# Optimization experiments

Measured on AMD Instinct MI355X. Metric: run time of the kernel, lower is better.

## Reference

```python
import jax, jax.numpy as jnp
import numpy as np

B, S, D = 1, 4096, 512
H, DK, DV = 8, 64, 64


def setup_inputs() -> dict:
    key = jax.random.key(0)
    ks = jax.random.split(key, 8)
    s = 1.0 / np.sqrt(D)
    return {
        "queries": jax.random.normal(ks[0], (B, S, D), jnp.float32),
        "keys": jax.random.normal(ks[1], (B, S, D), jnp.float32),
        "values": jax.random.normal(ks[2], (B, S, D), jnp.float32),
        # Linear weights stored as [in, out] for x @ W
        "Wq": jax.random.normal(ks[3], (D, H * DK), jnp.float32) * s,
        "Wk": jax.random.normal(ks[4], (D, H * DK), jnp.float32) * s,
        "Wv": jax.random.normal(ks[5], (D, H * DV), jnp.float32) * s,
        "Wo": jax.random.normal(ks[6], (H * DV, D), jnp.float32) * s,
        "bo": jax.random.normal(ks[7], (D,), jnp.float32) * 0.02,
    }


def reference(queries, keys, values, Wq, Wk, Wv, Wo, bo):
    b, qlen = values.shape[0], queries.shape[1]
    q = (queries @ Wq).reshape(b, qlen, H, DK)
    k = (keys @ Wk).reshape(b, keys.shape[1], H, DK)
    v = (values @ Wv).reshape(b, values.shape[1], H, DV)
    scale = DK ** 0.5
    # naive full attention: materialize [b, h, sq, sk] scores
    scores = jnp.einsum("bqhd,bkhd->bhqk", q, k) / scale
    attn = jax.nn.softmax(scores, axis=-1)
    out = jnp.einsum("bhqk,bkhd->bqhd", attn, v).reshape(b, qlen, H * DV)
    out = out @ Wo + bo          # first fc_out
    out = out @ Wo + bo          # second fc_out (module applies it twice when not reversible)
    return out
```

## Files before the change

### kernel.cpp

```cpp
#include <hip/hip_runtime.h>

#define S_LEN  4096
#define DMODEL 512
#define NH     8
#define HD     64

typedef _Float16 f16x8 __attribute__((ext_vector_type(8)));
typedef _Float16 f16x4 __attribute__((ext_vector_type(4)));
typedef float    f32x4 __attribute__((ext_vector_type(4)));

static __device__ __forceinline__ unsigned short f2h(float x) {
  return __builtin_bit_cast(unsigned short, (_Float16)x);
}

__global__ __launch_bounds__(256) void wtrans_kernel(
    const float* __restrict__ w0, const float* __restrict__ w1,
    const float* __restrict__ w2, const float* __restrict__ w3,
    unsigned short* __restrict__ o0, unsigned short* __restrict__ o1,
    unsigned short* __restrict__ o2, unsigned short* __restrict__ o3,
    unsigned short* __restrict__ o3s)
{
  __shared__ unsigned short T[64 * 72];
  const float* W; unsigned short* O;
  switch (blockIdx.z) {
    case 0:  W = w0; O = o0; break;
    case 1:  W = w1; O = o1; break;
    case 2:  W = w2; O = o2; break;
    default: W = w3; O = o3; break;
  }
  const int tid = threadIdx.x;
  const int k0 = blockIdx.x * 64, n0 = blockIdx.y * 64;
  const int c4 = (tid & 15) * 4;
#pragma unroll
  for (int rp = 0; rp < 4; ++rp) {
    int r = rp * 16 + (tid >> 4);
    float4 x = *(const float4*)(W + (k0 + r) * DMODEL + n0 + c4);
    T[(c4 + 0) * 72 + r] = f2h(x.x);
    T[(c4 + 1) * 72 + r] = f2h(x.y);
    T[(c4 + 2) * 72 + r] = f2h(x.z);
    T[(c4 + 3) * 72 + r] = f2h(x.w);
    if (blockIdx.z == 3) {
      f16x4 st;
      st[0] = (_Float16)x.x; st[1] = (_Float16)x.y;
      st[2] = (_Float16)x.z; st[3] = (_Float16)x.w;
      *(f16x4*)&o3s[(k0 + r) * DMODEL + n0 + c4] = st;
    }
  }
  __syncthreads();
#pragma unroll
  for (int it = 0; it < 2; ++it) {
    int i = tid + it * 256;
    int nl = i >> 3, c = i & 7;
    *(f16x8*)&O[(n0 + nl) * DMODEL + k0 + c * 8] = *(const f16x8*)&T[nl * 72 + c * 8];
  }
}

__global__ __launch_bounds__(256) void gemm128_kernel(
    const void* __restrict__ A0, const void* __restrict__ A1,
    const void* __restrict__ A2, const void* __restrict__ A3,
    const unsigned short* __restrict__ B0, const unsigned short* __restrict__ B1,
    const unsigned short* __restrict__ B2, const unsigned short* __restrict__ B3,
    void* __restrict__ C0, void* __restrict__ C1,
    void* __restrict__ C2, void* __restrict__ C3,
    const float* __restrict__ bias, unsigned short* __restrict__ vtg,
    const float* __restrict__ wo_f32, const float* __restrict__ bo_in,
    float* __restrict__ bo2_out,
    int a_fp32_mask, int c_fp32_mask)
{
  constexpr int K = DMODEL, N = DMODEL;
  __shared__ unsigned short As[128 * 32];
  __shared__ unsigned short Bs[128 * 32];
  const int z = blockIdx.z;
  if (z == 3 && blockIdx.x >= 4) {
    if (blockIdx.x < 12 && blockIdx.y == 0 && wo_f32) {
      int col = (blockIdx.x - 4) * 64 + (threadIdx.x & 63);
      float s = bo_in[col];
#pragma unroll 8
      for (int j = 0; j < DMODEL; ++j) s = fmaf(bo_in[j], wo_f32[j * DMODEL + col], s);
      bo2_out[col] = s;
    }
    return;
  }
  const void* Av; const unsigned short* Bt; void* Cv;
  switch (z) {
    case 0:  Av = A0; Bt = B0; Cv = C0; break;
    case 1:  Av = A1; Bt = B1; Cv = C1; break;
    case 2:  Av = A2; Bt = B2; Cv = C2; break;
    default: Av = A3; Bt = B3; Cv = C3; break;
  }
  const int a_fp32 = (a_fp32_mask >> z) & 1;
  const int c_fp32 = (c_fp32_mask >> z) & 1;
  const int tid  = threadIdx.x;
  const int lane = tid & 63;
  const int wid  = tid >> 6;
  const int quad = lane >> 4, l16 = lane & 15;
  const int m0 = blockIdx.x * 128, n0 = blockIdx.y * 128;
  const int wm = (wid >> 1) * 64, wn = (wid & 1) * 64;
  f32x4 acc[4][4] = {};

  f16x8 areg[2], breg[2];
#pragma unroll
  for (int it = 0; it < 2; ++it) {
    int s = it * 256 + tid;
    int r = s >> 2, ck = (s & 3) * 8;
    if (a_fp32) {
      const float* p = (const float*)Av + (m0 + r) * K + ck;
      float4 x = *(const float4*)p;
      float4 y = *(const float4*)(p + 4);
      f16x8 av;
      av[0] = (_Float16)x.x; av[1] = (_Float16)x.y;
      av[2] = (_Float16)x.z; av[3] = (_Float16)x.w;
      av[4] = (_Float16)y.x; av[5] = (_Float16)y.y;
      av[6] = (_Float16)y.z; av[7] = (_Float16)y.w;
      areg[it] = av;
    } else {
      areg[it] = *(const f16x8*)((const unsigned short*)Av + (m0 + r) * K + ck);
    }
    breg[it] = *(const f16x8*)(Bt + (n0 + r) * K + ck);
  }

  for (int k0 = 0; k0 < K; k0 += 32) {
    __syncthreads();
#pragma unroll
    for (int it = 0; it < 2; ++it) {
      int s = it * 256 + tid;
      int r = s >> 2, ck = (s & 3) * 8;
      *(f16x8*)&As[r * 32 + ck] = areg[it];
      *(f16x8*)&Bs[r * 32 + ck] = breg[it];
    }
    __syncthreads();

    if (k0 + 32 < K) {
      int kk = k0 + 32;
#pragma unroll
      for (int it = 0; it < 2; ++it) {
        int s = it * 256 + tid;
        int r = s >> 2, ck = (s & 3) * 8;
        if (a_fp32) {
          const float* p = (const float*)Av + (m0 + r) * K + kk + ck;
          float4 x = *(const float4*)p;
          float4 y = *(const float4*)(p + 4);
          f16x8 av;
          av[0] = (_Float16)x.x; av[1] = (_Float16)x.y;
          av[2] = (_Float16)x.z; av[3] = (_Float16)x.w;
          av[4] = (_Float16)y.x; av[5] = (_Float16)y.y;
          av[6] = (_Float16)y.z; av[7] = (_Float16)y.w;
          areg[it] = av;
        } else {
          areg[it] = *(const f16x8*)((const unsigned short*)Av + (m0 + r) * K + kk + ck);
        }
        breg[it] = *(const f16x8*)(Bt + (n0 + r) * K + kk + ck);
      }
    }

    f16x8 af[4], bf[4];
#pragma unroll
    for (int mt = 0; mt < 4; ++mt)
      af[mt] = *(const f16x8*)&As[(wm + mt * 16 + l16) * 32 + quad * 8];
#pragma unroll
    for (int nt = 0; nt < 4; ++nt)
      bf[nt] = *(const f16x8*)&Bs[(wn + nt * 16 + l16) * 32 + quad * 8];
#pragma unroll
    for (int mt = 0; mt < 4; ++mt)
#pragma unroll
      for (int nt = 0; nt < 4; ++nt)
        acc[mt][nt] = __builtin_amdgcn_mfma_f32_16x16x32_f16(af[mt], bf[nt], acc[mt][nt], 0, 0, 0);
  }

  const int do_vt = (vtg != nullptr) && (z == 2);
#pragma unroll
  for (int mt = 0; mt < 4; ++mt)
#pragma unroll
    for (int nt = 0; nt < 4; ++nt) {
      int col = n0 + wn + nt * 16 + l16;
      float bv = bias ? bias[col] : 0.f;
#pragma unroll
      for (int g = 0; g < 4; ++g) {
        int row = m0 + wm + mt * 16 + quad * 4 + g;
        float val = acc[mt][nt][g] + bv;
        if (do_vt)        vtg[col * S_LEN + row] = f2h(val);
        else if (c_fp32)  ((float*)Cv)[row * N + col] = val;
        else              ((unsigned short*)Cv)[row * N + col] = f2h(val);
      }
    }
}

__global__ __launch_bounds__(256) void attn_kernel(
    const unsigned short* __restrict__ Qb, const unsigned short* __restrict__ Kb,
    const unsigned short* __restrict__ VtG,
    float* __restrict__ P0, unsigned short* __restrict__ P1,
    float* __restrict__ mp, float* __restrict__ lp)
{
  __shared__ unsigned short Ks[64 * 72];
  __shared__ unsigned short Vt[64 * 64];

  const int tid  = threadIdx.x;
  const int lane = tid & 63;
  const int wid  = tid >> 6;
  const int quad = lane >> 4, l16 = lane & 15;
  const int qb = blockIdx.x, h = blockIdx.y, z = blockIdx.z;
  const int hc = h * HD;
  const int qbase = qb * 128 + wid * 32;
  const int kz = z * 2048;

  f16x8 bq[2][2];
#pragma unroll
  for (int s = 0; s < 2; ++s) {
    int qrow = qbase + s * 16 + l16;
    bq[s][0] = *(const f16x8*)(Qb + qrow * DMODEL + hc + quad * 8);
    bq[s][1] = *(const f16x8*)(Qb + qrow * DMODEL + hc + 32 + quad * 8);
  }

  f32x4 o[2][4] = {};
  float m_run[2] = {-1e30f, -1e30f}, l_run[2] = {0.f, 0.f};

  f16x8 kreg[2], vreg[2];
#pragma unroll
  for (int it = 0; it < 2; ++it) {
    int s = it * 256 + tid;
    int n = s >> 3, c = s & 7;
    kreg[it] = *(const f16x8*)(Kb + (kz + n) * DMODEL + hc + c * 8);
    vreg[it] = *(const f16x8*)(VtG + (hc + n) * S_LEN + kz + c * 8);
  }

  for (int kbi = 0; kbi < 32; ++kbi) {
    __syncthreads();
#pragma unroll
    for (int it = 0; it < 2; ++it) {
      int s = it * 256 + tid;
      int n = s >> 3, c = s & 7;
      *(f16x8*)&Ks[n * 72 + c * 8] = kreg[it];
      int vbase = n * 16;
      int n15 = n & 15;
      f16x4 lo = __builtin_shufflevector(vreg[it], vreg[it], 0, 1, 2, 3);
      f16x4 hi = __builtin_shufflevector(vreg[it], vreg[it], 4, 5, 6, 7);
      *(f16x4*)&Vt[(vbase + ((2 * c) ^ n15)) * 4]     = lo;
      *(f16x4*)&Vt[(vbase + ((2 * c + 1) ^ n15)) * 4] = hi;
    }
    __syncthreads();

    if (kbi + 1 < 32) {
      int kb1 = kz + (kbi + 1) * 64;
#pragma unroll
      for (int it = 0; it < 2; ++it) {
        int s = it * 256 + tid;
        int n = s >> 3, c = s & 7;
        kreg[it] = *(const f16x8*)(Kb + (kb1 + n) * DMODEL + hc + c * 8);
        vreg[it] = *(const f16x8*)(VtG + (hc + n) * S_LEN + kb1 + c * 8);
      }
    }

    f32x4 sT[2][4];
#pragma unroll
    for (int kt = 0; kt < 4; ++kt) {
      f16x8 ak0 = *(const f16x8*)&Ks[(kt * 16 + l16) * 72 + quad * 8];
      f16x8 ak1 = *(const f16x8*)&Ks[(kt * 16 + l16) * 72 + 32 + quad * 8];
#pragma unroll
      for (int s = 0; s < 2; ++s) {
        f32x4 a = {};
        a = __builtin_amdgcn_mfma_f32_16x16x32_f16(ak0, bq[s][0], a, 0, 0, 0);
        a = __builtin_amdgcn_mfma_f32_16x16x32_f16(ak1, bq[s][1], a, 0, 0, 0);
        sT[s][kt] = a;
      }
    }

    f16x4 pa[2][4];
#pragma unroll
    for (int s = 0; s < 2; ++s) {
      float vmax = -1e30f;
#pragma unroll
      for (int kt = 0; kt < 4; ++kt)
#pragma unroll
        for (int g = 0; g < 4; ++g) vmax = fmaxf(vmax, sT[s][kt][g]);
      vmax = fmaxf(vmax, __shfl_xor(vmax, 16));
      vmax = fmaxf(vmax, __shfl_xor(vmax, 32));

      if (__all(vmax <= m_run[s] + 8.0f)) {
        const float mn = m_run[s];
        float rs = 0.f;
#pragma unroll
        for (int kt = 0; kt < 4; ++kt)
#pragma unroll
          for (int g = 0; g < 4; ++g) {
            float p = __expf((sT[s][kt][g] - mn) * 0.125f);
            rs += p;
            pa[s][kt][g] = (_Float16)p;
          }
        rs += __shfl_xor(rs, 16);
        rs += __shfl_xor(rs, 32);
        l_run[s] += rs;
      } else {
        const float mn = fmaxf(m_run[s], vmax);
        const float alpha = __expf((m_run[s] - mn) * 0.125f);
        m_run[s] = mn;

        float rs = 0.f;
#pragma unroll
        for (int kt = 0; kt < 4; ++kt)
#pragma unroll
          for (int g = 0; g < 4; ++g) {
            float p = __expf((sT[s][kt][g] - mn) * 0.125f);
            rs += p;
            pa[s][kt][g] = (_Float16)p;
          }
        rs += __shfl_xor(rs, 16);
        rs += __shfl_xor(rs, 32);
        l_run[s] = l_run[s] * alpha + rs;

        float ag[4];
#pragma unroll
        for (int g = 0; g < 4; ++g) ag[g] = __shfl(alpha, quad * 4 + g);
#pragma unroll
        for (int nt = 0; nt < 4; ++nt)
#pragma unroll
          for (int g = 0; g < 4; ++g) o[s][nt][g] *= ag[g];
      }
    }

#pragma unroll
    for (int nt = 0; nt < 4; ++nt) {
      int dbase = (nt * 16 + l16) * 16;
#pragma unroll
      for (int kt = 0; kt < 4; ++kt) {
        f16x4 bv = *(const f16x4*)&Vt[(dbase + ((kt * 4 + quad) ^ l16)) * 4];
#pragma unroll
        for (int s = 0; s < 2; ++s)
          o[s][nt] = __builtin_amdgcn_mfma_f32_16x16x16f16(pa[s][kt], bv, o[s][nt], 0, 0, 0);
      }
    }
  }

#pragma unroll
  for (int s = 0; s < 2; ++s) {
    const float lt = l_run[s];
    const float rl = 1.f / lt;
    if (quad == 0) {
      int q = qbase + s * 16 + l16;
      mp[(z * NH + h) * S_LEN + q] = m_run[s];
      lp[(z * NH + h) * S_LEN + q] = lt;
    }
    float rlg[4];
#pragma unroll
    for (int g = 0; g < 4; ++g) rlg[g] = __shfl(rl, quad * 4 + g);
#pragma unroll
    for (int g = 0; g < 4; ++g) {
      int row = qbase + s * 16 + quad * 4 + g;
#pragma unroll
      for (int nt = 0; nt < 4; ++nt) {
        float val = o[s][nt][g] * rlg[g];
        if (z == 0) P0[row * DMODEL + hc + nt * 16 + l16] = val;
        else        P1[row * DMODEL + hc + nt * 16 + l16] = f2h(val);
      }
    }
  }
}

__global__ __launch_bounds__(256) void merge_kernel(
    const float* __restrict__ P0, const unsigned short* __restrict__ P1,
    const float* __restrict__ mp, const float* __restrict__ lp,
    unsigned short* __restrict__ Ob)
{
  const int tid = threadIdx.x;
  const int qb = blockIdx.x, h = blockIdx.y;
  const int q = qb * 64 + (tid >> 2), hc = h * HD;
  const int dq = (tid & 3) * 16;
  const float m0 = mp[h * S_LEN + q],        l0 = lp[h * S_LEN + q];
  const float m1 = mp[(NH + h) * S_LEN + q], l1 = lp[(NH + h) * S_LEN + q];
  const float M  = fmaxf(m0, m1);
  float w0 = l0 * __expf((m0 - M) * 0.125f);
  float w1 = l1 * __expf((m1 - M) * 0.125f);
  const float rw = 1.f / (w0 + w1);
  w0 *= rw; w1 *= rw;
  const int base = q * DMODEL + hc + dq;
  f16x8 p1a = *(const f16x8*)&P1[base];
  f16x8 p1b = *(const f16x8*)&P1[base + 8];
  float4 x0 = *(const float4*)&P0[base];
  float4 x1 = *(const float4*)&P0[base + 4];
  float4 x2 = *(const float4*)&P0[base + 8];
  float4 x3 = *(const float4*)&P0[base + 12];
  f16x8 oa, ob;
  oa[0] = (_Float16)(w0 * x0.x + w1 * (float)p1a[0]);
  oa[1] = (_Float16)(w0 * x0.y + w1 * (float)p1a[1]);
  oa[2] = (_Float16)(w0 * x0.z + w1 * (float)p1a[2]);
  oa[3] = (_Float16)(w0 * x0.w + w1 * (float)p1a[3]);
  oa[4] = (_Float16)(w0 * x1.x + w1 * (float)p1a[4]);
  oa[5] = (_Float16)(w0 * x1.y + w1 * (float)p1a[5]);
  oa[6] = (_Float16)(w0 * x1.z + w1 * (float)p1a[6]);
  oa[7] = (_Float16)(w0 * x1.w + w1 * (float)p1a[7]);
  ob[0] = (_Float16)(w0 * x2.x + w1 * (float)p1b[0]);
  ob[1] = (_Float16)(w0 * x2.y + w1 * (float)p1b[1]);
  ob[2] = (_Float16)(w0 * x2.z + w1 * (float)p1b[2]);
  ob[3] = (_Float16)(w0 * x2.w + w1 * (float)p1b[3]);
  ob[4] = (_Float16)(w0 * x3.x + w1 * (float)p1b[4]);
  ob[5] = (_Float16)(w0 * x3.y + w1 * (float)p1b[5]);
  ob[6] = (_Float16)(w0 * x3.z + w1 * (float)p1b[6]);
  ob[7] = (_Float16)(w0 * x3.w + w1 * (float)p1b[7]);
  *(f16x8*)&Ob[base]     = oa;
  *(f16x8*)&Ob[base + 8] = ob;
}

extern "C" void kernel_launch(void* const* d_in, const int* in_sizes, int n_in,
                              void* d_out, int out_size, void* d_ws, size_t ws_size,
                              hipStream_t stream) {
  const float* q  = (const float*)d_in[0];
  const float* k  = (const float*)d_in[1];
  const float* v  = (const float*)d_in[2];
  const float* Wq = (const float*)d_in[3];
  const float* Wk = (const float*)d_in[4];
  const float* Wv = (const float*)d_in[5];
  const float* Wo = (const float*)d_in[6];
  const float* bo = (const float*)d_in[7];

  unsigned short* ws   = (unsigned short*)d_ws;
  unsigned short* Wqt  = ws;
  unsigned short* Wkt  = Wqt  + 262144;
  unsigned short* Wvt  = Wkt  + 262144;
  unsigned short* Wot  = Wvt  + 262144;
  unsigned short* Wof  = Wot  + 262144;
  unsigned short* Wo2t = Wof  + 262144;
  unsigned short* Qb   = Wo2t + 262144;
  unsigned short* Kb   = Qb   + 2097152;
  unsigned short* VtG  = Kb   + 2097152;
  unsigned short* Ab   = VtG  + 2097152;
  float*          bo2  = (float*)(Ab + 2097152);
  float*          mp   = bo2 + 512;
  float*          lp   = mp + 65536;

  wtrans_kernel<<<dim3(8, 8, 4), 256, 0, stream>>>(
      Wq, Wk, Wv, Wo, Wqt, Wkt, Wvt, Wot, Wof);

  gemm128_kernel<<<dim3(32, 4, 4), 256, 0, stream>>>(
      q, k, v, Wot, Wqt, Wkt, Wvt, Wof, Qb, Kb, nullptr, Wo2t,
      nullptr, VtG, Wo, bo, bo2, 0x7, 0x0);

  attn_kernel<<<dim3(32, 8, 2), 256, 0, stream>>>(
      Qb, Kb, VtG, (float*)d_out, Ab, mp, lp);

  merge_kernel<<<dim3(64, 8), 256, 0, stream>>>(
      (const float*)d_out, Ab, mp, lp, Ab);

  gemm128_kernel<<<dim3(32, 4, 1), 256, 0, stream>>>(
      Ab, nullptr, nullptr, nullptr, Wo2t, nullptr, nullptr, nullptr,
      d_out, nullptr, nullptr, nullptr, bo2, nullptr,
      nullptr, nullptr, nullptr, 0x0, 0x1);
}
```

Measured before the change: 206.6 us.

## Double-buffer attention K/V tiles with direct global-to-LDS loads and XOR swizzle

Replaces the register-staged K/V tile loads in the attention kernel with global_load_lds (direct to LDS) into double-buffered shared tiles. It uses explicit vmcnt waits and raw barriers so the next tile's fetch overlaps the current tile's compute. The padded K layout and the old V swizzle become an XOR-swizzled 64-wide layout, removing register staging and LDS write instructions. The grid is flattened to 1D with heads and splits as the fast index to change block scheduling order, at the cost of hand-managed waitcnt correctness.

```diff
diff --git a/kernel.cpp b/kernel.cpp
--- a/kernel.cpp
+++ b/kernel.cpp
@@ -11,6 +11,12 @@
 
 static __device__ __forceinline__ unsigned short f2h(float x) {
   return __builtin_bit_cast(unsigned short, (_Float16)x);
+}
+
+static __device__ __forceinline__ void glds16(const void* g, void* l) {
+  __builtin_amdgcn_global_load_lds(
+      (const __attribute__((address_space(1))) void*)g,
+      (__attribute__((address_space(3))) void*)l, 16, 0, 0);
 }
 
 __global__ __launch_bounds__(256) void wtrans_kernel(
@@ -191,14 +197,17 @@
     float* __restrict__ P0, unsigned short* __restrict__ P1,
     float* __restrict__ mp, float* __restrict__ lp)
 {
-  __shared__ unsigned short Ks[64 * 72];
-  __shared__ unsigned short Vt[64 * 64];
+  __shared__ unsigned short Ks[2][64 * 64];
+  __shared__ unsigned short Vt[2][64 * 64];
 
   const int tid  = threadIdx.x;
   const int lane = tid & 63;
   const int wid  = tid >> 6;
   const int quad = lane >> 4, l16 = lane & 15;
-  const int qb = blockIdx.x, h = blockIdx.y, z = blockIdx.z;
+  const int id = blockIdx.x;
+  const int qb = id >> 4;
+  const int hz = id & 15;
+  const int h  = hz & 7, z = hz >> 3;
   const int hc = h * HD;
   const int qbase = qb * 128 + wid * 32;
   const int kz = z * 2048;
@@ -210,51 +219,53 @@
     bq[s][0] = *(const f16x8*)(Qb + qrow * DMODEL + hc + quad * 8);
     bq[s][1] = *(const f16x8*)(Qb + qrow * DMODEL + hc + 32 + quad * 8);
   }
+  asm volatile("" : "+v"(bq[0][0]), "+v"(bq[0][1]), "+v"(bq[1][0]), "+v"(bq[1][1]));
 
   f32x4 o[2][4] = {};
   float m_run[2] = {-1e30f, -1e30f}, l_run[2] = {0.f, 0.f};
 
-  f16x8 kreg[2], vreg[2];
-#pragma unroll
-  for (int it = 0; it < 2; ++it) {
-    int s = it * 256 + tid;
-    int n = s >> 3, c = s & 7;
-    kreg[it] = *(const f16x8*)(Kb + (kz + n) * DMODEL + hc + c * 8);
-    vreg[it] = *(const f16x8*)(VtG + (hc + n) * S_LEN + kz + c * 8);
-  }
+  const unsigned short *kp0, *kp1, *vp0, *vp1;
+  {
+    int s0 = tid, s1 = 256 + tid;
+    int n0 = s0 >> 3, c0 = (s0 & 7) ^ (n0 & 7);
+    int n1 = s1 >> 3, c1 = (s1 & 7) ^ (n1 & 7);
+    kp0 = Kb + (kz + n0) * DMODEL + hc + c0 * 8;
+    kp1 = Kb + (kz + n1) * DMODEL + hc + c1 * 8;
+    vp0 = VtG + (hc + n0) * S_LEN + kz + c0 * 8;
+    vp1 = VtG + (hc + n1) * S_LEN + kz + c1 * 8;
+  }
+
+  glds16(kp0, &Ks[0][tid * 8]);
+  glds16(kp1, &Ks[0][(256 + tid) * 8]);
+  glds16(vp0, &Vt[0][tid * 8]);
+  glds16(vp1, &Vt[0][(256 + tid) * 8]);
 
   for (int kbi = 0; kbi < 32; ++kbi) {
-    __syncthreads();
-#pragma unroll
-    for (int it = 0; it < 2; ++it) {
-      int s = it * 256 + tid;
-      int n = s >> 3, c = s & 7;
-      *(f16x8*)&Ks[n * 72 + c * 8] = kreg[it];
-      int vbase = n * 16;
-      int n15 = n & 15;
-      f16x4 lo = __builtin_shufflevector(vreg[it], vreg[it], 0, 1, 2, 3);
-      f16x4 hi = __builtin_shufflevector(vreg[it], vreg[it], 4, 5, 6, 7);
-      *(f16x4*)&Vt[(vbase + ((2 * c) ^ n15)) * 4]     = lo;
-      *(f16x4*)&Vt[(vbase + ((2 * c + 1) ^ n15)) * 4] = hi;
-    }
-    __syncthreads();
-
+    const int cur = kbi & 1;
+    __builtin_amdgcn_s_barrier();
     if (kbi + 1 < 32) {
-      int kb1 = kz + (kbi + 1) * 64;
-#pragma unroll
-      for (int it = 0; it < 2; ++it) {
-        int s = it * 256 + tid;
-        int n = s >> 3, c = s & 7;
-        kreg[it] = *(const f16x8*)(Kb + (kb1 + n) * DMODEL + hc + c * 8);
-        vreg[it] = *(const f16x8*)(VtG + (hc + n) * S_LEN + kb1 + c * 8);
-      }
-    }
+      const int t = kbi + 1;
+      glds16(kp0 + t * (64 * DMODEL), &Ks[cur ^ 1][tid * 8]);
+      glds16(kp1 + t * (64 * DMODEL), &Ks[cur ^ 1][(256 + tid) * 8]);
+      glds16(vp0 + t * 64,            &Vt[cur ^ 1][tid * 8]);
+      glds16(vp1 + t * 64,            &Vt[cur ^ 1][(256 + tid) * 8]);
+      asm volatile("s_waitcnt vmcnt(4)" ::: "memory");
+    } else {
+      asm volatile("s_waitcnt vmcnt(0)" ::: "memory");
+    }
+    __builtin_amdgcn_s_barrier();
+    asm volatile("" ::: "memory");
+
+    const unsigned short* KsC = Ks[cur];
+    const unsigned short* VtC = Vt[cur];
 
     f32x4 sT[2][4];
 #pragma unroll
     for (int kt = 0; kt < 4; ++kt) {
-      f16x8 ak0 = *(const f16x8*)&Ks[(kt * 16 + l16) * 72 + quad * 8];
-      f16x8 ak1 = *(const f16x8*)&Ks[(kt * 16 + l16) * 72 + 32 + quad * 8];
+      int r = kt * 16 + l16;
+      int sw = l16 & 7;
+      f16x8 ak0 = *(const f16x8*)&KsC[r * 64 + ((quad    ) ^ sw) * 8];
+      f16x8 ak1 = *(const f16x8*)&KsC[r * 64 + ((quad + 4) ^ sw) * 8];
 #pragma unroll
       for (int s = 0; s < 2; ++s) {
         f32x4 a = {};
@@ -319,10 +330,12 @@
 
 #pragma unroll
     for (int nt = 0; nt < 4; ++nt) {
-      int dbase = (nt * 16 + l16) * 16;
+      int d = nt * 16 + l16;
+      int sw = l16 & 7;
 #pragma unroll
       for (int kt = 0; kt < 4; ++kt) {
-        f16x4 bv = *(const f16x4*)&Vt[(dbase + ((kt * 4 + quad) ^ l16)) * 4];
+        int u = kt * 4 + quad;
+        f16x4 bv = *(const f16x4*)&VtC[d * 64 + (((u >> 1) ^ sw) * 8) + (u & 1) * 4];
 #pragma unroll
         for (int s = 0; s < 2; ++s)
           o[s][nt] = __builtin_amdgcn_mfma_f32_16x16x16f16(pa[s][kt], bv, o[s][nt], 0, 0, 0);
@@ -433,7 +446,7 @@
       q, k, v, Wot, Wqt, Wkt, Wvt, Wof, Qb, Kb, nullptr, Wo2t,
       nullptr, VtG, Wo, bo, bo2, 0x7, 0x0);
 
-  attn_kernel<<<dim3(32, 8, 2), 256, 0, stream>>>(
+  attn_kernel<<<dim3(512), 256, 0, stream>>>(
       Qb, Kb, VtG, (float*)d_out, Ab, mp, lp);
 
   merge_kernel<<<dim3(64, 8), 256, 0, stream>>>(
```

Result: faster. 201.5 us (-2.5%).
